# Performance work log

Hardware: AMD Instinct MI355X
Metric: run time of the kernel (lower is better)

## Reference

```python
import jax, jax.numpy as jnp
import numpy as np

KEYS = 11     # inference_keys: number of heatmap channels / keypoints
NSTACK = 4
B, H, W = 16, 128, 128


def setup_inputs() -> dict:
    key = jax.random.key(0)
    k1, k2, k3 = jax.random.split(key, 3)
    combined_preds = jax.random.normal(k1, (B, NSTACK, 2 * KEYS, H, W), dtype=jnp.float32)
    heatmaps = jax.random.uniform(k2, (B, KEYS, H, W), dtype=jnp.float32)
    # labels[..., 9] and [..., 10] are keypoint coords; scale to [0, 160) so some
    # fall outside [0, H)=[0,128) and exercise the validity-mask branch.
    labels = jax.random.uniform(k3, (B, KEYS, 11), dtype=jnp.float32) * 160.0
    return {"combined_preds": combined_preds, "heatmaps": heatmaps, "labels": labels}


def reference(combined_preds, heatmaps, labels):
    keys = KEYS
    hm = combined_preds[:, :, :keys]          # [B, S, K, H, W] heatmap preds
    lb = combined_preds[:, :, keys:]          # [B, S, K, H, W] label preds
    b, s, k, m, n = hm.shape                  # m = H, n = W (code uses m for both // and %)

    # HeatmapLoss per stack, vectorized over the stack dim
    heat_loss = ((hm - heatmaps[:, None]) ** 2).sum(axis=(2, 3, 4))  # [B, S]

    # LabelLoss, fully vectorized over (B, S, K)
    flat = hm.reshape(b, s, k, m * n)
    index = jnp.argmax(flat, axis=-1)         # [B, S, K]
    x = index // m                            # matches int(index / m) in original
    y = index % m
    # a[x, y] where a is the [H, W] heatmap -> flat[x * W + y]
    a_xy = jnp.take_along_axis(flat, (x * n + y)[..., None], axis=-1)[..., 0]

    pred = lb.reshape(b, s, k, -1)            # [B, S, K, H*W]
    lab = labels[:, None]                     # [B, 1, K, 11] broadcast over stacks

    gx, gy = lab[..., 9], lab[..., 10]
    valid = (gx > 0) & (gy > 0) & (gx < m) & (gy < n)

    xf = x.astype(pred.dtype)
    yf = y.astype(pred.dtype)
    xy_loss = (gx + lab[..., 7] - xf - pred[..., 7]) ** 2 \
            + (gy + lab[..., 8] - yf - pred[..., 8]) ** 2
    conf_loss = (1.0 - a_xy) ** 2
    class_loss = ((pred[..., 0:7] - lab[..., 0:7]) ** 2).sum(axis=-1)

    per_kp = jnp.where(valid, class_loss + xy_loss + conf_loss, 0.0)  # [B, S, K]
    label_loss = per_kp.sum(axis=-1)                                   # [B, S]

    return heat_loss, label_loss
```

## Files before the change

### kernel.cpp

```cpp
#include <hip/hip_runtime.h>
#include <math.h>

#define KEYS 11
#define NSTACK 4
#define NB 16
#define HH 128
#define WW 128
#define HW (HH * WW)
#define NGRP (NB * KEYS)
#define NCHUNK 4
#define CF4 (HW / 4 / NCHUNK)

typedef float f4 __attribute__((ext_vector_type(4)));

#define WS_SUM 0
#define WS_V   (NGRP * NCHUNK * NSTACK)
#define WS_I   (2 * NGRP * NCHUNK * NSTACK)

__global__ __launch_bounds__(256) void kp_main(
    const float* __restrict__ cp,
    const float* __restrict__ heat,
    float* __restrict__ ws)
{
    const int bid = blockIdx.x;
    const int c   = bid & (NCHUNK - 1);
    const int grp = bid >> 2;
    const int b = grp / KEYS;
    const int k = grp % KEYS;
    const int tid = threadIdx.x;

    const int coff = c * CF4;
    const f4* __restrict__ ht4 = (const f4*)(heat + (size_t)grp * HW) + coff;
    const f4* __restrict__ hm0 = (const f4*)(cp + ((size_t)((b * NSTACK + 0) * (2 * KEYS) + k)) * HW) + coff;
    const f4* __restrict__ hm1 = (const f4*)(cp + ((size_t)((b * NSTACK + 1) * (2 * KEYS) + k)) * HW) + coff;
    const f4* __restrict__ hm2 = (const f4*)(cp + ((size_t)((b * NSTACK + 2) * (2 * KEYS) + k)) * HW) + coff;
    const f4* __restrict__ hm3 = (const f4*)(cp + ((size_t)((b * NSTACK + 3) * (2 * KEYS) + k)) * HW) + coff;

    float sum[NSTACK]  = {0.0f, 0.0f, 0.0f, 0.0f};
    float vmax[NSTACK] = {-INFINITY, -INFINITY, -INFINITY, -INFINITY};
    int   imax[NSTACK] = {0, 0, 0, 0};

    #pragma unroll
    for (int i = tid; i < CF4; i += 256) {
        f4 cv = __builtin_nontemporal_load(ht4 + i);
        f4 a[NSTACK];
        a[0] = __builtin_nontemporal_load(hm0 + i);
        a[1] = __builtin_nontemporal_load(hm1 + i);
        a[2] = __builtin_nontemporal_load(hm2 + i);
        a[3] = __builtin_nontemporal_load(hm3 + i);
        const int base = (coff + i) * 4;
        #pragma unroll
        for (int s = 0; s < NSTACK; ++s) {
            float d0 = a[s][0] - cv[0], d1 = a[s][1] - cv[1];
            float d2 = a[s][2] - cv[2], d3 = a[s][3] - cv[3];
            sum[s] += d0 * d0 + d1 * d1 + d2 * d2 + d3 * d3;
            if (a[s][0] > vmax[s]) { vmax[s] = a[s][0]; imax[s] = base;     }
            if (a[s][1] > vmax[s]) { vmax[s] = a[s][1]; imax[s] = base + 1; }
            if (a[s][2] > vmax[s]) { vmax[s] = a[s][2]; imax[s] = base + 2; }
            if (a[s][3] > vmax[s]) { vmax[s] = a[s][3]; imax[s] = base + 3; }
        }
    }

    #pragma unroll
    for (int off = 32; off > 0; off >>= 1) {
        #pragma unroll
        for (int s = 0; s < NSTACK; ++s) {
            float ov = __shfl_down(vmax[s], off);
            int   oi = __shfl_down(imax[s], off);
            float os = __shfl_down(sum[s],  off);
            sum[s] += os;
            if (ov > vmax[s] || (ov == vmax[s] && oi < imax[s])) { vmax[s] = ov; imax[s] = oi; }
        }
    }

    __shared__ float s_sum[4][NSTACK];
    __shared__ float s_v[4][NSTACK];
    __shared__ int   s_i[4][NSTACK];
    const int wave = tid >> 6;
    if ((tid & 63) == 0) {
        #pragma unroll
        for (int s = 0; s < NSTACK; ++s) {
            s_sum[wave][s] = sum[s]; s_v[wave][s] = vmax[s]; s_i[wave][s] = imax[s];
        }
    }
    __syncthreads();

    if (tid < NSTACK) {
        const int s = tid;
        float fsum = s_sum[0][s];
        float fv   = s_v[0][s];
        int   fi   = s_i[0][s];
        #pragma unroll
        for (int w = 1; w < 4; w++) {
            fsum += s_sum[w][s];
            if (s_v[w][s] > fv || (s_v[w][s] == fv && s_i[w][s] < fi)) {
                fv = s_v[w][s]; fi = s_i[w][s];
            }
        }
        const int idx = (grp * NCHUNK + c) * NSTACK + s;
        ws[WS_SUM + idx] = fsum;
        ws[WS_V   + idx] = fv;
        ws[WS_I   + idx] = __int_as_float(fi);
    }
}

__global__ __launch_bounds__(768) void kp_final(
    const float* __restrict__ cp,
    const float* __restrict__ lab,
    const float* __restrict__ ws,
    float* __restrict__ out)
{
    __shared__ float sh[NGRP * NSTACK];
    __shared__ float sl[NGRP * NSTACK];
    const int t = threadIdx.x;

    if (t < NGRP * NSTACK) {
        const int g = t >> 2;
        const int s = t & 3;
        const int b = g / KEYS;
        const int k = g % KEYS;

        float fsum = 0.0f;
        float fv   = -INFINITY;
        int   fi   = 0;
        #pragma unroll
        for (int c = 0; c < NCHUNK; ++c) {
            const int idx = (g * NCHUNK + c) * NSTACK + s;
            float ps = ws[WS_SUM + idx];
            float pv = ws[WS_V   + idx];
            int   pi = __float_as_int(ws[WS_I + idx]);
            fsum += ps;
            if (pv > fv || (pv == fv && pi < fi)) { fv = pv; fi = pi; }
        }
        sh[t] = fsum;

        const float* __restrict__ lb = cp + ((size_t)((b * NSTACK + s) * (2 * KEYS) + KEYS + k)) * HW;
        const float* __restrict__ L  = lab + (size_t)g * 11;
        float gx = L[9], gy = L[10];
        bool valid = (gx > 0.0f) && (gy > 0.0f) && (gx < (float)HH) && (gy < (float)WW);
        float loss = 0.0f;
        if (valid) {
            float xf = (float)(fi / WW);
            float yf = (float)(fi % WW);
            float dx = gx + L[7] - xf - lb[7];
            float dy = gy + L[8] - yf - lb[8];
            loss = dx * dx + dy * dy;
            float cm = 1.0f - fv;
            loss += cm * cm;
            #pragma unroll
            for (int j = 0; j < 7; j++) {
                float d = lb[j] - L[j];
                loss += d * d;
            }
        }
        sl[t] = loss;
    }
    __syncthreads();

    if (t < NB * NSTACK) {
        const int b = t / NSTACK;
        const int s = t % NSTACK;
        float h = 0.0f, l = 0.0f;
        #pragma unroll
        for (int k = 0; k < KEYS; ++k) {
            const int g = b * KEYS + k;
            h += sh[g * NSTACK + s];
            l += sl[g * NSTACK + s];
        }
        out[t] = h;
        out[64 + t] = l;
    }
}

extern "C" void kernel_launch(void* const* d_in, const int* in_sizes, int n_in,
                              void* d_out, int out_size, void* d_ws, size_t ws_size,
                              hipStream_t stream) {
    const float* cp   = (const float*)d_in[0];
    const float* heat = (const float*)d_in[1];
    const float* lab  = (const float*)d_in[2];
    float* out = (float*)d_out;
    float* ws  = (float*)d_ws;

    kp_main<<<NGRP * NCHUNK, 256, 0, stream>>>(cp, heat, ws);
    kp_final<<<1, 768, 0, stream>>>(cp, lab, ws, out);
}
```

Measured before the change: 134.0 us.

## Fuse main and final kernels via cooperative grid sync, precompute label terms

Merges the partial-reduction kernel and the single-block finalize kernel into one cooperative launch that uses a grid-wide barrier, removing the second kernel launch and its gap. Label-loss inputs (class loss, offsets, validity) are precomputed by chunk-0 blocks, and per-chunk partials are packed into float4 records so the final block does fewer scattered loads. The occupancy check multiplies per-CU blocks by 256 CUs, and the code falls back to two launches if it fails. A grid sync adds its own barrier cost and requires all 704 blocks to be co-resident.

```diff
diff --git a/kernel.cpp b/kernel.cpp
--- a/kernel.cpp
+++ b/kernel.cpp
@@ -1,5 +1,8 @@
 #include <hip/hip_runtime.h>
+#include <hip/hip_cooperative_groups.h>
 #include <math.h>
+
+namespace cg = cooperative_groups;
 
 #define KEYS 11
 #define NSTACK 4
@@ -10,24 +13,21 @@
 #define NGRP (NB * KEYS)
 #define NCHUNK 4
 #define CF4 (HW / 4 / NCHUNK)
+#define NBLK (NGRP * NCHUNK)
 
 typedef float f4 __attribute__((ext_vector_type(4)));
 
-#define WS_SUM 0
-#define WS_V   (NGRP * NCHUNK * NSTACK)
-#define WS_I   (2 * NGRP * NCHUNK * NSTACK)
-
-__global__ __launch_bounds__(256) void kp_main(
-    const float* __restrict__ cp,
-    const float* __restrict__ heat,
-    float* __restrict__ ws)
-{
-    const int bid = blockIdx.x;
+#define WS_LP (NBLK * NSTACK * 4)
+
+__device__ __forceinline__ void do_chunk(
+    const float* __restrict__ cp, const float* __restrict__ heat,
+    const float* __restrict__ lab, float* __restrict__ ws,
+    int bid, int tid)
+{
     const int c   = bid & (NCHUNK - 1);
     const int grp = bid >> 2;
     const int b = grp / KEYS;
     const int k = grp % KEYS;
-    const int tid = threadIdx.x;
 
     const int coff = c * CF4;
     const f4* __restrict__ ht4 = (const f4*)(heat + (size_t)grp * HW) + coff;
@@ -97,69 +97,69 @@
                 fv = s_v[w][s]; fi = s_i[w][s];
             }
         }
-        const int idx = (grp * NCHUNK + c) * NSTACK + s;
-        ws[WS_SUM + idx] = fsum;
-        ws[WS_V   + idx] = fv;
-        ws[WS_I   + idx] = __int_as_float(fi);
-    }
-}
-
-__global__ __launch_bounds__(768) void kp_final(
-    const float* __restrict__ cp,
-    const float* __restrict__ lab,
-    const float* __restrict__ ws,
-    float* __restrict__ out)
+        f4 rec; rec[0] = fsum; rec[1] = fv; rec[2] = __int_as_float(fi); rec[3] = 0.0f;
+        ((f4*)ws)[(size_t)(grp * NSTACK + s) * NCHUNK + c] = rec;
+
+        if (c == 0) {
+            const float* __restrict__ lb = cp + ((size_t)((b * NSTACK + s) * (2 * KEYS) + KEYS + k)) * HW;
+            const float* __restrict__ L  = lab + (size_t)grp * 11;
+            float gx = L[9], gy = L[10];
+            bool valid = (gx > 0.0f) && (gy > 0.0f) && (gx < (float)HH) && (gy < (float)WW);
+            float cls = 0.0f;
+            #pragma unroll
+            for (int j = 0; j < 7; j++) {
+                float d = lb[j] - L[j];
+                cls += d * d;
+            }
+            f4 a; a[0] = gx + L[7]; a[1] = gy + L[8]; a[2] = lb[7]; a[3] = lb[8];
+            f4 bb; bb[0] = cls; bb[1] = valid ? 1.0f : 0.0f; bb[2] = 0.0f; bb[3] = 0.0f;
+            f4* lp = (f4*)(ws + WS_LP);
+            lp[(size_t)(grp * NSTACK + s) * 2 + 0] = a;
+            lp[(size_t)(grp * NSTACK + s) * 2 + 1] = bb;
+        }
+    }
+}
+
+__device__ __forceinline__ void do_final(
+    const float* __restrict__ ws, float* __restrict__ out, int tid)
 {
     __shared__ float sh[NGRP * NSTACK];
     __shared__ float sl[NGRP * NSTACK];
-    const int t = threadIdx.x;
-
-    if (t < NGRP * NSTACK) {
-        const int g = t >> 2;
-        const int s = t & 3;
-        const int b = g / KEYS;
-        const int k = g % KEYS;
-
-        float fsum = 0.0f;
-        float fv   = -INFINITY;
-        int   fi   = 0;
+
+    for (int idx = tid; idx < NGRP * NSTACK; idx += 256) {
+        const f4* pr = (const f4*)ws + (size_t)idx * NCHUNK;
+        float fsum = 0.0f, fv = -INFINITY;
+        int   fi = 0;
         #pragma unroll
         for (int c = 0; c < NCHUNK; ++c) {
-            const int idx = (g * NCHUNK + c) * NSTACK + s;
-            float ps = ws[WS_SUM + idx];
-            float pv = ws[WS_V   + idx];
-            int   pi = __float_as_int(ws[WS_I + idx]);
-            fsum += ps;
+            f4 r = pr[c];
+            fsum += r[0];
+            float pv = r[1];
+            int   pi = __float_as_int(r[2]);
             if (pv > fv || (pv == fv && pi < fi)) { fv = pv; fi = pi; }
         }
-        sh[t] = fsum;
-
-        const float* __restrict__ lb = cp + ((size_t)((b * NSTACK + s) * (2 * KEYS) + KEYS + k)) * HW;
-        const float* __restrict__ L  = lab + (size_t)g * 11;
-        float gx = L[9], gy = L[10];
-        bool valid = (gx > 0.0f) && (gy > 0.0f) && (gx < (float)HH) && (gy < (float)WW);
+        sh[idx] = fsum;
+
+        const f4* lp = (const f4*)(ws + WS_LP) + (size_t)idx * 2;
+        f4 a = lp[0], bb = lp[1];
         float loss = 0.0f;
-        if (valid) {
+        if (bb[1] != 0.0f) {
             float xf = (float)(fi / WW);
             float yf = (float)(fi % WW);
-            float dx = gx + L[7] - xf - lb[7];
-            float dy = gy + L[8] - yf - lb[8];
+            float dx = (a[0] - xf) - a[2];
+            float dy = (a[1] - yf) - a[3];
             loss = dx * dx + dy * dy;
             float cm = 1.0f - fv;
             loss += cm * cm;
-            #pragma unroll
-            for (int j = 0; j < 7; j++) {
-                float d = lb[j] - L[j];
-                loss += d * d;
-            }
-        }
-        sl[t] = loss;
+            loss += bb[0];
+        }
+        sl[idx] = loss;
     }
     __syncthreads();
 
-    if (t < NB * NSTACK) {
-        const int b = t / NSTACK;
-        const int s = t % NSTACK;
+    if (tid < NB * NSTACK) {
+        const int b = tid >> 2;
+        const int s = tid & 3;
         float h = 0.0f, l = 0.0f;
         #pragma unroll
         for (int k = 0; k < KEYS; ++k) {
@@ -167,9 +167,32 @@
             h += sh[g * NSTACK + s];
             l += sl[g * NSTACK + s];
         }
-        out[t] = h;
-        out[64 + t] = l;
-    }
+        out[tid] = h;
+        out[64 + tid] = l;
+    }
+}
+
+__global__ __launch_bounds__(256, 3) void kp_fused(
+    const float* __restrict__ cp, const float* __restrict__ heat,
+    const float* __restrict__ lab, float* __restrict__ ws, float* __restrict__ out)
+{
+    do_chunk(cp, heat, lab, ws, blockIdx.x, threadIdx.x);
+    __threadfence();
+    cg::this_grid().sync();
+    if (blockIdx.x == 0) do_final(ws, out, threadIdx.x);
+}
+
+__global__ __launch_bounds__(256) void kp_main2(
+    const float* __restrict__ cp, const float* __restrict__ heat,
+    const float* __restrict__ lab, float* __restrict__ ws)
+{
+    do_chunk(cp, heat, lab, ws, blockIdx.x, threadIdx.x);
+}
+
+__global__ __launch_bounds__(256) void kp_final2(
+    const float* __restrict__ ws, float* __restrict__ out)
+{
+    do_final(ws, out, threadIdx.x);
 }
 
 extern "C" void kernel_launch(void* const* d_in, const int* in_sizes, int n_in,
@@ -181,6 +204,20 @@
     float* out = (float*)d_out;
     float* ws  = (float*)d_ws;
 
-    kp_main<<<NGRP * NCHUNK, 256, 0, stream>>>(cp, heat, ws);
-    kp_final<<<1, 768, 0, stream>>>(cp, lab, ws, out);
-}
+    static int use_coop = -1;
+    if (use_coop < 0) {
+        int maxb = 0;
+        hipError_t e = hipOccupancyMaxActiveBlocksPerMultiprocessor(&maxb, kp_fused, 256, 0);
+        use_coop = (e == hipSuccess && maxb * 256 >= NBLK) ? 1 : 0;
+    }
+    if (use_coop) {
+        void* args[] = {(void*)&cp, (void*)&heat, (void*)&lab, (void*)&ws, (void*)&out};
+        hipError_t e = hipLaunchCooperativeKernel((const void*)kp_fused,
+                                                  dim3(NBLK), dim3(256), args, 0, stream);
+        if (e != hipSuccess) use_coop = 0;
+    }
+    if (!use_coop) {
+        kp_main2<<<NBLK, 256, 0, stream>>>(cp, heat, lab, ws);
+        kp_final2<<<1, 256, 0, stream>>>(ws, out);
+    }
+}
```

Result: slower. 230.4 us (+71.9%).
